# Performance work log

Measured on AMD Instinct MI355X. Metric: run time of the kernel, lower is better.

Reference implementation:

```python
import jax, jax.numpy as jnp
import numpy as np

NEG = -1e12


def setup_inputs() -> dict:
    key = jax.random.key(0)
    ks = jax.random.split(key, 6)
    B, S, D, H = 32, 2048, 1024, 1024  # batch, seq, dec/enc dim, hidden
    last_state = jax.random.normal(ks[0], (B, D), dtype=jnp.float32)
    enc_outputs = jax.random.normal(ks[1], (B, S, D), dtype=jnp.float32)
    attn_masks = jax.random.randint(ks[2], (B, S), 0, 2, dtype=jnp.int32)
    W = jax.random.normal(ks[3], (H, 2 * D), dtype=jnp.float32) * 0.02
    b = jax.random.normal(ks[4], (H,), dtype=jnp.float32) * 0.02
    V = jax.random.normal(ks[5], (H,), dtype=jnp.float32)
    return {"last_state": last_state, "enc_outputs": enc_outputs,
            "attn_masks": attn_masks, "W": W, "b": b, "V": V}


def reference(last_state, enc_outputs, attn_masks, W, b, V):
    # Split W to avoid materializing the [B,S,2D] concat:
    # concat([h, e]) @ W.T == h @ Wh.T + e @ We.T
    D = last_state.shape[-1]
    Wh, We = W[:, :D], W[:, D:]
    # hidden part: [B,H], broadcast over seq
    h_part = jnp.einsum('bd,hd->bh', last_state, Wh)  # [B,H]
    e_part = jnp.einsum('bsd,hd->bsh', enc_outputs, We)  # [B,S,H]
    sim = jnp.tanh(h_part[:, None, :] + e_part + b)  # [B,S,H]
    scores = jnp.einsum('bsh,h->bs', sim, V)  # [B,S]
    scores = jnp.where(attn_masks != 1, jnp.float32(NEG), scores)
    attn_weights = jax.nn.softmax(scores, axis=1)  # [B,S]
    context = jnp.einsum('bs,bsd->bd', attn_weights, enc_outputs)  # [B,D]
    return context, attn_weights, scores
```

## Files before the change

kernel.cpp:

```cpp
#include <hip/hip_runtime.h>
#include <math.h>
#include <stdint.h>

#define B_ 32
#define S_ 2048
#define D_ 1024
#define H_ 1024
#define NEGV -1000000000000.0f

typedef __attribute__((ext_vector_type(8))) short bf16x8;
typedef __attribute__((ext_vector_type(8))) _Float16 f16x8;
typedef __attribute__((ext_vector_type(4))) float f32x4;

static __device__ __forceinline__ unsigned short f2bf(float x) {
    union { float f; unsigned u; } v; v.f = x;
    unsigned r = v.u + 0x7FFF + ((v.u >> 16) & 1);
    return (unsigned short)(r >> 16);
}
static __device__ __forceinline__ float bf2f(unsigned short h) {
    union { float f; unsigned u; } v; v.u = ((unsigned)h) << 16; return v.f;
}
static __device__ __forceinline__ unsigned short f2h(float x) {
    _Float16 h = (_Float16)x; unsigned short u;
    __builtin_memcpy(&u, &h, 2); return u;
}
static __device__ __forceinline__ float h2f(unsigned short u) {
    _Float16 h; __builtin_memcpy(&h, &u, 2); return (float)h;
}
static __device__ __forceinline__ float tanh_fast(float x) {
    float e = __expf(2.f * x);
    return 1.f - 2.f / (e + 1.f);
}
static __device__ __forceinline__ void gl_lds16(unsigned short* lds, const unsigned short* g) {
    __builtin_amdgcn_global_load_lds(
        (const __attribute__((address_space(1))) unsigned int*)(const void*)g,
        (__attribute__((address_space(3))) unsigned int*)(void*)lds,
        16, 0, 0);
}

__global__ __launch_bounds__(256) void k_W_f16(const float* __restrict__ W,
                                               unsigned short* __restrict__ out) {
    int idx = blockIdx.x * 256 + threadIdx.x;
    int h = idx >> 7, kc = idx & 127;
    const float* src = W + (size_t)h * (2 * D_) + D_ + kc * 8;
    float4 a = *(const float4*)src;
    float4 c4 = *(const float4*)(src + 4);
    float v[8] = {a.x, a.y, a.z, a.w, c4.x, c4.y, c4.z, c4.w};
    unsigned short t[8];
#pragma unroll
    for (int j = 0; j < 8; ++j) t[j] = f2h(v[j]);
    uint4 w;
    w.x = t[0] | ((unsigned)t[1] << 16); w.y = t[2] | ((unsigned)t[3] << 16);
    w.z = t[4] | ((unsigned)t[5] << 16); w.w = t[6] | ((unsigned)t[7] << 16);
    int g = kc >> 3, cc = kc & 7;
    int dst = g * 64 + ((cc ^ (h & 7)) << 3);
    *(uint4*)(out + (size_t)h * D_ + dst) = w;
}

__global__ __launch_bounds__(256) void k_hpart(const float* __restrict__ ls,
                                               const float* __restrict__ W,
                                               float* __restrict__ hp) {
    int bh = blockIdx.x * 256 + threadIdx.x;
    int b = bh >> 10, h = bh & 1023;
    const float* lsr = ls + b * D_;
    const float* wr  = W + (size_t)h * (2 * D_);
    float acc = 0.f;
#pragma unroll 4
    for (int d = 0; d < D_; d += 4) {
        float4 a = *(const float4*)(lsr + d);
        float4 w = *(const float4*)(wr + d);
        acc += a.x * w.x + a.y * w.y + a.z * w.z + a.w * w.w;
    }
    hp[bh] = acc;
}

__global__ __launch_bounds__(512, 2) void k_scores_fused(
    const float* __restrict__ enc,
    const unsigned short* __restrict__ Wf16,
    const float* __restrict__ hp, const float* __restrict__ bias,
    const float* __restrict__ V, float* __restrict__ spart)
{
    extern __shared__ unsigned short smem[];
    unsigned short* smemA = smem;
    unsigned short* smemB = smem + 32768;

    const int tid  = threadIdx.x;
    const int lane = tid & 63, wid = tid >> 6;
    const int wm = wid >> 2, wn = wid & 3;
    const int l15 = lane & 15, lhi = lane >> 4;

    const int bid  = blockIdx.x;
    const int wgid = (bid & 7) * 128 + (bid >> 3);
    const int mt = wgid >> 2, nt = wgid & 3;
    const int m0 = mt * 256;
    const int nt256 = nt * 256;
    const int b = m0 >> 11;

    const size_t boff = (size_t)(nt256 + wid * 16 + (lane >> 3)) * D_ + (lane & 7) * 8;
    const int ldsw = wid * 1024;

    f32x4 acc[8][4];
#pragma unroll
    for (int i = 0; i < 8; ++i)
#pragma unroll
        for (int j = 0; j < 4; ++j)
            acc[i][j] = (f32x4){0.f, 0.f, 0.f, 0.f};

    const int swz = l15 & 7;

    float4 ar0[4], ar1[4];

#define LOAD_A(KOFS) do {                                                           \
    _Pragma("unroll")                                                               \
    for (int s_ = 0; s_ < 4; ++s_) {                                                \
        int p_ = tid + s_ * 512;                                                    \
        int row_ = p_ >> 3, pc_ = p_ & 7;                                           \
        const float* ap_ = enc + (size_t)(m0 + row_) * D_ + (KOFS) + pc_ * 8;       \
        ar0[s_] = *(const float4*)ap_;                                              \
        ar1[s_] = *(const float4*)(ap_ + 4);                                        \
    }                                                                               \
} while (0)
#define WRITE_A(SLOT) do {                                                          \
    _Pragma("unroll")                                                               \
    for (int s_ = 0; s_ < 4; ++s_) {                                                \
        int p_ = tid + s_ * 512;                                                    \
        int row_ = p_ >> 3, pc_ = p_ & 7;                                           \
        float v_[8] = {ar0[s_].x, ar0[s_].y, ar0[s_].z, ar0[s_].w,                  \
                       ar1[s_].x, ar1[s_].y, ar1[s_].z, ar1[s_].w};                 \
        unsigned short t_[8];                                                       \
        _Pragma("unroll")                                                           \
        for (int j_ = 0; j_ < 8; ++j_) t_[j_] = f2h(v_[j_]);                        \
        uint4 w_;                                                                   \
        w_.x = t_[0] | ((unsigned)t_[1] << 16); w_.y = t_[2] | ((unsigned)t_[3] << 16); \
        w_.z = t_[4] | ((unsigned)t_[5] << 16); w_.w = t_[6] | ((unsigned)t_[7] << 16); \
        *(uint4*)&smemA[(SLOT) * 16384 + row_ * 64 + ((pc_ ^ (row_ & 7)) << 3)] = w_; \
    }                                                                               \
} while (0)

#define STAGE_B(SLOT, HALF, KOFS) do {                                              \
    unsigned short* d_ = &smemB[(SLOT) * 16384 + (HALF) * 8192 + ldsw];             \
    const unsigned short* s_ = Wf16 + boff + (size_t)(HALF) * 131072 + (KOFS);      \
    gl_lds16(d_, s_);                                                               \
    gl_lds16(d_ + 512, s_ + 8192);                                                  \
} while (0)

#define LDA(AR, CUR, MH, KS) do {                                                   \
    _Pragma("unroll")                                                               \
    for (int fi_ = 0; fi_ < 4; ++fi_) {                                             \
        int row_ = wm * 128 + (MH) * 64 + fi_ * 16 + l15;                           \
        int ch_  = ((KS) * 4 + lhi) ^ swz;                                          \
        AR[fi_] = *(const f16x8*)&smemA[(CUR) * 16384 + row_ * 64 + ch_ * 8];       \
    }                                                                               \
} while (0)
#define LDB(BR, CUR, KS) do {                                                       \
    _Pragma("unroll")                                                               \
    for (int fi_ = 0; fi_ < 4; ++fi_) {                                             \
        int row_ = wn * 64 + fi_ * 16 + l15;                                        \
        int ch_  = ((KS) * 4 + lhi) ^ swz;                                          \
        BR[fi_] = *(const f16x8*)&smemB[(CUR) * 16384 + row_ * 64 + ch_ * 8];       \
    }                                                                               \
} while (0)
#define MFMA16(AR, BR, MH) do {                                                     \
    __builtin_amdgcn_s_setprio(1);                                                  \
    _Pragma("unroll")                                                               \
    for (int fi_ = 0; fi_ < 4; ++fi_)                                               \
    _Pragma("unroll")                                                               \
        for (int fj_ = 0; fj_ < 4; ++fj_)                                           \
            acc[(MH) * 4 + fi_][fj_] = __builtin_amdgcn_mfma_f32_16x16x32_f16(      \
                AR[fi_], BR[fj_], acc[(MH) * 4 + fi_][fj_], 0, 0, 0);               \
    __builtin_amdgcn_s_setprio(0);                                                  \
} while (0)

    LOAD_A(0);
    STAGE_B(0, 0, 0);
    STAGE_B(0, 1, 0);
    WRITE_A(0);
    __syncthreads();

    f16x8 a[4], bk[4];
#pragma unroll 1
    for (int t = 0; t < 16; ++t) {
        const int cur = t & 1, nxt = cur ^ 1;
        const int kofs = (t + 1) * 64;

        if (t < 15) {
            LOAD_A(kofs);
            STAGE_B(nxt, 0, kofs);
            STAGE_B(nxt, 1, kofs);
        }

#pragma unroll
        for (int ks = 0; ks < 2; ++ks) {
            LDB(bk, cur, ks);
            LDA(a, cur, 0, ks);
            MFMA16(a, bk, 0);
            LDA(a, cur, 1, ks);
            MFMA16(a, bk, 1);
        }

        if (t < 15) WRITE_A(nxt);

        __syncthreads();
    }

    float hb[4], vv[4];
#pragma unroll
    for (int fn = 0; fn < 4; ++fn) {
        int h = nt256 + wn * 64 + fn * 16 + l15;
        hb[fn] = hp[b * H_ + h] + bias[h];
        vv[fn] = V[h];
    }
    float* s_red = (float*)smem;
#pragma unroll
    for (int fm = 0; fm < 8; ++fm)
#pragma unroll
        for (int rg = 0; rg < 4; ++rg) {
            float rs = 0.f;
#pragma unroll
            for (int fn = 0; fn < 4; ++fn)
                rs += tanh_fast(acc[fm][fn][rg] + hb[fn]) * vv[fn];
            rs += __shfl_xor(rs, 1, 16);
            rs += __shfl_xor(rs, 2, 16);
            rs += __shfl_xor(rs, 4, 16);
            rs += __shfl_xor(rs, 8, 16);
            if (l15 == 0)
                s_red[wid * 128 + fm * 16 + lhi * 4 + rg] = rs;
        }
    __syncthreads();
    if (tid < 256) {
        int wmr = tid >> 7, rr = tid & 127;
        float v = s_red[(wmr * 4 + 0) * 128 + rr] + s_red[(wmr * 4 + 1) * 128 + rr]
                + s_red[(wmr * 4 + 2) * 128 + rr] + s_red[(wmr * 4 + 3) * 128 + rr];
        spart[(size_t)nt * 65536 + m0 + tid] = v;
    }
#undef LOAD_A
#undef WRITE_A
#undef STAGE_B
#undef LDA
#undef LDB
#undef MFMA16
}

__global__ __launch_bounds__(256) void k_softmax_fold(const float* __restrict__ spart,
                                                      const int* __restrict__ mask,
                                                      float* __restrict__ scores_out,
                                                      float* __restrict__ weights) {
    __shared__ float red[8];
    int b = blockIdx.x, tid = threadIdx.x;
    float vals[8];
    float mx = -INFINITY;
#pragma unroll
    for (int i = 0; i < 8; ++i) {
        int m = b * S_ + tid + i * 256;
        float s = spart[m] + spart[65536 + m] + spart[131072 + m] + spart[196608 + m];
        s = (mask[m] == 1) ? s : NEGV;
        scores_out[m] = s;
        vals[i] = s;
        mx = fmaxf(mx, s);
    }
    for (int off = 32; off; off >>= 1) mx = fmaxf(mx, __shfl_xor(mx, off, 64));
    int wave = tid >> 6;
    if ((tid & 63) == 0) red[wave] = mx;
    __syncthreads();
    mx = fmaxf(fmaxf(red[0], red[1]), fmaxf(red[2], red[3]));
    float sum = 0.f;
#pragma unroll
    for (int i = 0; i < 8; ++i) {
        vals[i] = expf(vals[i] - mx);
        sum += vals[i];
    }
    for (int off = 32; off; off >>= 1) sum += __shfl_xor(sum, off, 64);
    if ((tid & 63) == 0) red[4 + wave] = sum;
    __syncthreads();
    sum = red[4] + red[5] + red[6] + red[7];
    float inv = 1.f / sum;
#pragma unroll
    for (int i = 0; i < 8; ++i)
        weights[b * S_ + tid + i * 256] = vals[i] * inv;
}

__global__ __launch_bounds__(256) void k_ctx_partial_f32(const float* __restrict__ weights,
                                                         const float* __restrict__ enc,
                                                         float* __restrict__ part) {
    int b = blockIdx.x >> 4;
    int chunk = blockIdx.x & 15;
    int tid = threadIdx.x;
    int d0 = tid * 4;
    float4 acc = {0.f, 0.f, 0.f, 0.f};
    int s0 = chunk * 128;
    const float* wrow = weights + b * S_;
    for (int s = s0; s < s0 + 128; ++s) {
        float w = wrow[s];
        if (w != 0.f) {
            float4 e = *(const float4*)(enc + (size_t)(b * S_ + s) * D_ + d0);
            acc.x += w * e.x; acc.y += w * e.y; acc.z += w * e.z; acc.w += w * e.w;
        }
    }
    *(float4*)(part + (size_t)blockIdx.x * D_ + d0) = acc;
}

__global__ __launch_bounds__(256) void k_ctx_reduce(const float* __restrict__ part,
                                                    float* __restrict__ ctx) {
    int bd = blockIdx.x * 256 + threadIdx.x;
    int b = bd >> 10, d = bd & 1023;
    float acc = 0.f;
#pragma unroll
    for (int c = 0; c < 16; ++c)
        acc += part[(size_t)(b * 16 + c) * D_ + d];
    ctx[bd] = acc;
}

__global__ __launch_bounds__(256) void k_splitW_lin(const float* __restrict__ W,
                                                    unsigned short* __restrict__ hi,
                                                    unsigned short* __restrict__ lo) {
    int idx = blockIdx.x * 256 + threadIdx.x;
    int h = idx >> 7, kc = idx & 127;
    const float* src = W + (size_t)h * (2 * D_) + D_ + kc * 8;
    float4 a = *(const float4*)src;
    float4 c = *(const float4*)(src + 4);
    float v[8] = {a.x, a.y, a.z, a.w, c.x, c.y, c.z, c.w};
    unsigned short th[8], tl[8];
#pragma unroll
    for (int j = 0; j < 8; ++j) {
        th[j] = f2bf(v[j]);
        tl[j] = f2bf(v[j] - bf2f(th[j]));
    }
    uint4 hw, lw;
    hw.x = th[0] | ((unsigned)th[1] << 16); hw.y = th[2] | ((unsigned)th[3] << 16);
    hw.z = th[4] | ((unsigned)th[5] << 16); hw.w = th[6] | ((unsigned)th[7] << 16);
    lw.x = tl[0] | ((unsigned)tl[1] << 16); lw.y = tl[2] | ((unsigned)tl[3] << 16);
    lw.z = tl[4] | ((unsigned)tl[5] << 16); lw.w = tl[6] | ((unsigned)tl[7] << 16);
    *(uint4*)(hi + (size_t)h * D_ + kc * 8) = hw;
    *(uint4*)(lo + (size_t)h * D_ + kc * 8) = lw;
}

__global__ __launch_bounds__(256, 2) void k_scores_mfma_fb(
    const float* __restrict__ enc,
    const unsigned short* __restrict__ Whi,
    const unsigned short* __restrict__ Wlo,
    const float* __restrict__ hp,
    const float* __restrict__ bias,
    const float* __restrict__ V,
    const int* __restrict__ mask,
    float* __restrict__ scores_out)
{
    __shared__ __align__(16) unsigned short smem[4 * 8192];
    unsigned short* sAhi = smem;
    unsigned short* sAlo = smem + 8192;
    unsigned short* sBhi = smem + 16384;
    unsigned short* sBlo = smem + 24576;

    const int tid  = threadIdx.x;
    const int lane = tid & 63, wid = tid >> 6;
    const int wr = wid >> 1, wc = wid & 1;
    const int l15 = lane & 15, lhi = lane >> 4;
    const int m0 = blockIdx.x * 128;
    const int b  = m0 >> 11;

    float rowsum[4][4] = {};
    float4 pa[8];
    uint4  pbh[4], pbl[4];

#define STAGE_LOAD(NB, KB) do {                                            \
    _Pragma("unroll")                                                      \
    for (int i_ = 0; i_ < 4; ++i_) {                                       \
        int c_ = tid + i_ * 256;                                           \
        int r_ = c_ >> 3, kc_ = c_ & 7;                                    \
        const float* ap_ = enc + (size_t)(m0 + r_) * D_ + (KB) * 64 + kc_ * 8; \
        pa[2 * i_]     = *(const float4*)ap_;                              \
        pa[2 * i_ + 1] = *(const float4*)(ap_ + 4);                        \
        size_t bo_ = (size_t)((NB) * 128 + r_) * D_ + (KB) * 64 + kc_ * 8; \
        pbh[i_] = *(const uint4*)(Whi + bo_);                              \
        pbl[i_] = *(const uint4*)(Wlo + bo_);                              \
    }                                                                      \
} while (0)

#define STAGE_WRITE() do {                                                 \
    _Pragma("unroll")                                                      \
    for (int i_ = 0; i_ < 4; ++i_) {                                       \
        int c_ = tid + i_ * 256;                                           \
        int sc_ = c_ ^ ((c_ >> 3) & 7);                                    \
        float vv_[8] = {pa[2*i_].x, pa[2*i_].y, pa[2*i_].z, pa[2*i_].w,    \
                        pa[2*i_+1].x, pa[2*i_+1].y, pa[2*i_+1].z, pa[2*i_+1].w}; \
        unsigned short th_[8], tl_[8];                                     \
        _Pragma("unroll")                                                  \
        for (int j_ = 0; j_ < 8; ++j_) {                                   \
            th_[j_] = f2bf(vv_[j_]);                                       \
            tl_[j_] = f2bf(vv_[j_] - bf2f(th_[j_]));                       \
        }                                                                  \
        uint4 hw_, lw_;                                                    \
        hw_.x = th_[0] | ((unsigned)th_[1] << 16); hw_.y = th_[2] | ((unsigned)th_[3] << 16); \
        hw_.z = th_[4] | ((unsigned)th_[5] << 16); hw_.w = th_[6] | ((unsigned)th_[7] << 16); \
        lw_.x = tl_[0] | ((unsigned)tl_[1] << 16); lw_.y = tl_[2] | ((unsigned)tl_[3] << 16); \
        lw_.z = tl_[4] | ((unsigned)tl_[5] << 16); lw_.w = tl_[6] | ((unsigned)tl_[7] << 16); \
        *(uint4*)&sAhi[sc_ * 8] = hw_;                                     \
        *(uint4*)&sAlo[sc_ * 8] = lw_;                                     \
        *(uint4*)&sBhi[sc_ * 8] = pbh[i_];                                 \
        *(uint4*)&sBlo[sc_ * 8] = pbl[i_];                                 \
    }                                                                      \
} while (0)

    STAGE_LOAD(0, 0);

    for (int nb = 0; nb < 8; ++nb) {
        f32x4 acc[4][4];
#pragma unroll
        for (int i = 0; i < 4; ++i)
#pragma unroll
            for (int j = 0; j < 4; ++j)
                acc[i][j] = (f32x4){0.f, 0.f, 0.f, 0.f};

        for (int kb = 0; kb < 16; ++kb) {
            __syncthreads();
            STAGE_WRITE();
            __syncthreads();
            int nkb = kb + 1, nnb = nb;
            if (nkb == 16) { nkb = 0; nnb = nb + 1; }
            if (nnb < 8) STAGE_LOAD(nnb, nkb);

#pragma unroll
            for (int ks = 0; ks < 2; ++ks) {
                bf16x8 bh[4], bl[4];
#pragma unroll
                for (int fn = 0; fn < 4; ++fn) {
                    int rB = wc * 64 + fn * 16 + l15;
                    int ch = (rB * 8 + ks * 4 + lhi) ^ (rB & 7);
                    bh[fn] = *(const bf16x8*)&sBhi[ch * 8];
                    bl[fn] = *(const bf16x8*)&sBlo[ch * 8];
                }
#pragma unroll
                for (int fm = 0; fm < 4; ++fm) {
                    int rA = wr * 64 + fm * 16 + l15;
                    int ch = (rA * 8 + ks * 4 + lhi) ^ (rA & 7);
                    bf16x8 ah = *(const bf16x8*)&sAhi[ch * 8];
                    bf16x8 al = *(const bf16x8*)&sAlo[ch * 8];
#pragma unroll
                    for (int fn = 0; fn < 4; ++fn) {
                        acc[fm][fn] = __builtin_amdgcn_mfma_f32_16x16x32_bf16(ah, bh[fn], acc[fm][fn], 0, 0, 0);
                        acc[fm][fn] = __builtin_amdgcn_mfma_f32_16x16x32_bf16(ah, bl[fn], acc[fm][fn], 0, 0, 0);
                        acc[fm][fn] = __builtin_amdgcn_mfma_f32_16x16x32_bf16(al, bh[fn], acc[fm][fn], 0, 0, 0);
                    }
                }
            }
        }

        int n0 = nb * 128;
#pragma unroll
        for (int fn = 0; fn < 4; ++fn) {
            int n = n0 + wc * 64 + fn * 16 + l15;
            float hbv = hp[b * H_ + n] + bias[n];
            float vvv = V[n];
#pragma unroll
            for (int fm = 0; fm < 4; ++fm) {
                f32x4 a = acc[fm][fn];
#pragma unroll
                for (int rg = 0; rg < 4; ++rg)
                    rowsum[fm][rg] += tanh_fast(a[rg] + hbv) * vvv;
            }
        }
    }

    __syncthreads();
    float* s_red = (float*)smem;
#pragma unroll
    for (int fm = 0; fm < 4; ++fm)
#pragma unroll
        for (int rg = 0; rg < 4; ++rg) {
            float v = rowsum[fm][rg];
            v += __shfl_xor(v, 1, 16);
            v += __shfl_xor(v, 2, 16);
            v += __shfl_xor(v, 4, 16);
            v += __shfl_xor(v, 8, 16);
            if (l15 == 0)
                s_red[wc * 128 + wr * 64 + fm * 16 + lhi * 4 + rg] = v;
        }
    __syncthreads();
    if (tid < 128) {
        int m = m0 + tid;
        float sc = s_red[tid] + s_red[128 + tid];
        scores_out[m] = (mask[m] == 1) ? sc : NEGV;
    }
#undef STAGE_LOAD
#undef STAGE_WRITE
}

__global__ __launch_bounds__(256) void k_softmax(const float* __restrict__ scores,
                                                 float* __restrict__ weights) {
    __shared__ float red[8];
    int b = blockIdx.x;
    int tid = threadIdx.x;
    const float* srow = scores + b * S_;
    float vals[8];
    float mx = -INFINITY;
#pragma unroll
    for (int i = 0; i < 8; ++i) {
        vals[i] = srow[tid + i * 256];
        mx = fmaxf(mx, vals[i]);
    }
    for (int off = 32; off; off >>= 1) mx = fmaxf(mx, __shfl_xor(mx, off, 64));
    int wave = tid >> 6;
    if ((tid & 63) == 0) red[wave] = mx;
    __syncthreads();
    mx = fmaxf(fmaxf(red[0], red[1]), fmaxf(red[2], red[3]));
    float sum = 0.f;
#pragma unroll
    for (int i = 0; i < 8; ++i) {
        vals[i] = expf(vals[i] - mx);
        sum += vals[i];
    }
    for (int off = 32; off; off >>= 1) sum += __shfl_xor(sum, off, 64);
    if ((tid & 63) == 0) red[4 + wave] = sum;
    __syncthreads();
    sum = red[4] + red[5] + red[6] + red[7];
    float inv = 1.f / sum;
#pragma unroll
    for (int i = 0; i < 8; ++i)
        weights[b * S_ + tid + i * 256] = vals[i] * inv;
}

extern "C" void kernel_launch(void* const* d_in, const int* in_sizes, int n_in,
                              void* d_out, int out_size, void* d_ws, size_t ws_size,
                              hipStream_t stream) {
    const float* ls   = (const float*)d_in[0];
    const float* enc  = (const float*)d_in[1];
    const int*   mask = (const int*)d_in[2];
    const float* W    = (const float*)d_in[3];
    const float* bias = (const float*)d_in[4];
    const float* V    = (const float*)d_in[5];

    float* out     = (float*)d_out;
    float* ctx     = out;
    float* weights = out + 32768;
    float* scores  = out + 98304;

    const size_t need = 2097152ull + 131072ull + 1048576ull + 2097152ull;

    if (ws_size >= need) {
        unsigned short* Wf16 = (unsigned short*)d_ws;
        float* hp    = (float*)(Wf16 + 1048576);
        float* spart = hp + 32768;
        float* part  = spart + 262144;

        hipFuncSetAttribute((const void*)k_scores_fused,
                            hipFuncAttributeMaxDynamicSharedMemorySize, 131072);

        k_W_f16<<<512, 256, 0, stream>>>(W, Wf16);
        k_hpart<<<128, 256, 0, stream>>>(ls, W, hp);
        k_scores_fused<<<1024, 512, 131072, stream>>>(enc, Wf16, hp, bias, V, spart);
        k_softmax_fold<<<32, 256, 0, stream>>>(spart, mask, scores, weights);
        k_ctx_partial_f32<<<512, 256, 0, stream>>>(weights, enc, part);
        k_ctx_reduce<<<128, 256, 0, stream>>>(part, ctx);
    } else {
        unsigned short* Whi = (unsigned short*)d_ws;
        unsigned short* Wlo = Whi + 1048576;
        float* hp   = (float*)(Wlo + 1048576);
        float* part = hp + 32768;

        k_splitW_lin<<<512, 256, 0, stream>>>(W, Whi, Wlo);
        k_hpart<<<128, 256, 0, stream>>>(ls, W, hp);
        k_scores_mfma_fb<<<512, 256, 0, stream>>>(enc, Whi, Wlo, hp, bias, V, mask, scores);
        k_softmax<<<32, 256, 0, stream>>>(scores, weights);
        k_ctx_partial_f32<<<512, 256, 0, stream>>>(weights, enc, part);
        k_ctx_reduce<<<128, 256, 0, stream>>>(part, ctx);
    }
}
```

Before: 256.7 us.

## Restructure scores GEMM into four-phase pipeline with fragment-major LDS layout

The fused scores GEMM main loop is split into four phases. Each phase interleaves LDS fragment reads, global loads of the next A tile, async B staging and MFMA groups, separated by explicit s_barrier, lgkmcnt and vmcnt waits. LDS now holds A and B in a fragment-major layout with no swizzle, so the W conversion kernel writes a linear layout. The goal is to hide global latency behind MFMA work and spread the LDS writes across the loop. The cost is many more barriers per iteration and possible LDS bank conflicts without the XOR swizzle.

```diff
diff --git a/kernel.cpp b/kernel.cpp
--- a/kernel.cpp
+++ b/kernel.cpp
@@ -38,8 +38,8 @@
         16, 0, 0);
 }
 
-__global__ __launch_bounds__(256) void k_W_f16(const float* __restrict__ W,
-                                               unsigned short* __restrict__ out) {
+__global__ __launch_bounds__(256) void k_W_f16_lin(const float* __restrict__ W,
+                                                   unsigned short* __restrict__ out) {
     int idx = blockIdx.x * 256 + threadIdx.x;
     int h = idx >> 7, kc = idx & 127;
     const float* src = W + (size_t)h * (2 * D_) + D_ + kc * 8;
@@ -52,9 +52,7 @@
     uint4 w;
     w.x = t[0] | ((unsigned)t[1] << 16); w.y = t[2] | ((unsigned)t[3] << 16);
     w.z = t[4] | ((unsigned)t[5] << 16); w.w = t[6] | ((unsigned)t[7] << 16);
-    int g = kc >> 3, cc = kc & 7;
-    int dst = g * 64 + ((cc ^ (h & 7)) << 3);
-    *(uint4*)(out + (size_t)h * D_ + dst) = w;
+    *(uint4*)(out + (size_t)h * D_ + kc * 8) = w;
 }
 
 __global__ __launch_bounds__(256) void k_hpart(const float* __restrict__ ls,
@@ -74,7 +72,7 @@
     hp[bh] = acc;
 }
 
-__global__ __launch_bounds__(512, 2) void k_scores_fused(
+__global__ __launch_bounds__(512, 2) void k_scores_4ph(
     const float* __restrict__ enc,
     const unsigned short* __restrict__ Wf16,
     const float* __restrict__ hp, const float* __restrict__ bias,
@@ -96,8 +94,9 @@
     const int nt256 = nt * 256;
     const int b = m0 >> 11;
 
-    const size_t boff = (size_t)(nt256 + wid * 16 + (lane >> 3)) * D_ + (lane & 7) * 8;
-    const int ldsw = wid * 1024;
+    const int arow_base = m0 + wm * 128 + wn * 32;
+    const int brg = wn * 4 + wm * 2;
+    const size_t bsrc_base = (size_t)(nt256 + brg * 16 + l15) * D_ + lhi * 8;
 
     f32x4 acc[8][4];
 #pragma unroll
@@ -106,59 +105,44 @@
         for (int j = 0; j < 4; ++j)
             acc[i][j] = (f32x4){0.f, 0.f, 0.f, 0.f};
 
-    const int swz = l15 & 7;
-
     float4 ar0[4], ar1[4];
 
-#define LOAD_A(KOFS) do {                                                           \
+#define LOAD_A1(S, KOFS) do {                                                       \
+    const float* ap_ = enc + (size_t)(arow_base + ((S) & 1) * 16 + l15) * D_        \
+                     + (KOFS) + (((S) >> 1) * 4 + lhi) * 8;                         \
+    ar0[S] = *(const float4*)ap_;                                                   \
+    ar1[S] = *(const float4*)(ap_ + 4);                                             \
+} while (0)
+#define WRITE_A1(S, SLOT) do {                                                      \
+    float v_[8] = {ar0[S].x, ar0[S].y, ar0[S].z, ar0[S].w,                          \
+                   ar1[S].x, ar1[S].y, ar1[S].z, ar1[S].w};                         \
+    unsigned short t_[8];                                                           \
     _Pragma("unroll")                                                               \
-    for (int s_ = 0; s_ < 4; ++s_) {                                                \
-        int p_ = tid + s_ * 512;                                                    \
-        int row_ = p_ >> 3, pc_ = p_ & 7;                                           \
-        const float* ap_ = enc + (size_t)(m0 + row_) * D_ + (KOFS) + pc_ * 8;       \
-        ar0[s_] = *(const float4*)ap_;                                              \
-        ar1[s_] = *(const float4*)(ap_ + 4);                                        \
-    }                                                                               \
-} while (0)
-#define WRITE_A(SLOT) do {                                                          \
-    _Pragma("unroll")                                                               \
-    for (int s_ = 0; s_ < 4; ++s_) {                                                \
-        int p_ = tid + s_ * 512;                                                    \
-        int row_ = p_ >> 3, pc_ = p_ & 7;                                           \
-        float v_[8] = {ar0[s_].x, ar0[s_].y, ar0[s_].z, ar0[s_].w,                  \
-                       ar1[s_].x, ar1[s_].y, ar1[s_].z, ar1[s_].w};                 \
-        unsigned short t_[8];                                                       \
-        _Pragma("unroll")                                                           \
-        for (int j_ = 0; j_ < 8; ++j_) t_[j_] = f2h(v_[j_]);                        \
-        uint4 w_;                                                                   \
-        w_.x = t_[0] | ((unsigned)t_[1] << 16); w_.y = t_[2] | ((unsigned)t_[3] << 16); \
-        w_.z = t_[4] | ((unsigned)t_[5] << 16); w_.w = t_[6] | ((unsigned)t_[7] << 16); \
-        *(uint4*)&smemA[(SLOT) * 16384 + row_ * 64 + ((pc_ ^ (row_ & 7)) << 3)] = w_; \
-    }                                                                               \
-} while (0)
-
-#define STAGE_B(SLOT, HALF, KOFS) do {                                              \
-    unsigned short* d_ = &smemB[(SLOT) * 16384 + (HALF) * 8192 + ldsw];             \
-    const unsigned short* s_ = Wf16 + boff + (size_t)(HALF) * 131072 + (KOFS);      \
-    gl_lds16(d_, s_);                                                               \
-    gl_lds16(d_ + 512, s_ + 8192);                                                  \
+    for (int j_ = 0; j_ < 8; ++j_) t_[j_] = f2h(v_[j_]);                            \
+    uint4 w_;                                                                       \
+    w_.x = t_[0] | ((unsigned)t_[1] << 16); w_.y = t_[2] | ((unsigned)t_[3] << 16); \
+    w_.z = t_[4] | ((unsigned)t_[5] << 16); w_.w = t_[6] | ((unsigned)t_[7] << 16); \
+    *(uint4*)&smemA[(SLOT) * 16384 + (wm * 8 + wn * 2 + ((S) & 1)) * 1024           \
+                    + (((S) >> 1) * 4 + lhi) * 128 + l15 * 8] = w_;                 \
+} while (0)
+#define STAGE_B(SLOT, KS, KOFS) do {                                                \
+    gl_lds16(&smemB[(SLOT) * 16384 + brg * 1024 + (KS) * 512],                      \
+             Wf16 + bsrc_base + (KOFS) + (KS) * 32);                                \
+    gl_lds16(&smemB[(SLOT) * 16384 + (brg + 1) * 1024 + (KS) * 512],                \
+             Wf16 + bsrc_base + 16 * D_ + (KOFS) + (KS) * 32);                      \
 } while (0)
 
 #define LDA(AR, CUR, MH, KS) do {                                                   \
     _Pragma("unroll")                                                               \
-    for (int fi_ = 0; fi_ < 4; ++fi_) {                                             \
-        int row_ = wm * 128 + (MH) * 64 + fi_ * 16 + l15;                           \
-        int ch_  = ((KS) * 4 + lhi) ^ swz;                                          \
-        AR[fi_] = *(const f16x8*)&smemA[(CUR) * 16384 + row_ * 64 + ch_ * 8];       \
-    }                                                                               \
+    for (int fi_ = 0; fi_ < 4; ++fi_)                                               \
+        AR[fi_] = *(const f16x8*)&smemA[(CUR) * 16384                               \
+            + (wm * 8 + (MH) * 4 + fi_) * 1024 + ((KS) * 4 + lhi) * 128 + l15 * 8]; \
 } while (0)
 #define LDB(BR, CUR, KS) do {                                                       \
     _Pragma("unroll")                                                               \
-    for (int fi_ = 0; fi_ < 4; ++fi_) {                                             \
-        int row_ = wn * 64 + fi_ * 16 + l15;                                        \
-        int ch_  = ((KS) * 4 + lhi) ^ swz;                                          \
-        BR[fi_] = *(const f16x8*)&smemB[(CUR) * 16384 + row_ * 64 + ch_ * 8];       \
-    }                                                                               \
+    for (int fi_ = 0; fi_ < 4; ++fi_)                                               \
+        BR[fi_] = *(const f16x8*)&smemB[(CUR) * 16384                               \
+            + (wn * 4 + fi_) * 1024 + ((KS) * 4 + lhi) * 128 + l15 * 8];            \
 } while (0)
 #define MFMA16(AR, BR, MH) do {                                                     \
     __builtin_amdgcn_s_setprio(1);                                                  \
@@ -171,10 +155,16 @@
     __builtin_amdgcn_s_setprio(0);                                                  \
 } while (0)
 
-    LOAD_A(0);
+#define BARRIER() asm volatile("s_barrier" ::: "memory")
+#define LGKM0()  do { asm volatile("s_waitcnt lgkmcnt(0)" ::: "memory");            \
+                      __builtin_amdgcn_sched_barrier(0); } while (0)
+#define VMC(N)   do { asm volatile("s_waitcnt vmcnt(" #N ")" ::: "memory");         \
+                      __builtin_amdgcn_sched_barrier(0); } while (0)
+
+    LOAD_A1(0, 0); LOAD_A1(1, 0); LOAD_A1(2, 0); LOAD_A1(3, 0);
+    WRITE_A1(0, 0); WRITE_A1(1, 0); WRITE_A1(2, 0); WRITE_A1(3, 0);
     STAGE_B(0, 0, 0);
     STAGE_B(0, 1, 0);
-    WRITE_A(0);
     __syncthreads();
 
     f16x8 a[4], bk[4];
@@ -182,25 +172,37 @@
     for (int t = 0; t < 16; ++t) {
         const int cur = t & 1, nxt = cur ^ 1;
         const int kofs = (t + 1) * 64;
-
-        if (t < 15) {
-            LOAD_A(kofs);
-            STAGE_B(nxt, 0, kofs);
-            STAGE_B(nxt, 1, kofs);
-        }
-
-#pragma unroll
-        for (int ks = 0; ks < 2; ++ks) {
-            LDB(bk, cur, ks);
-            LDA(a, cur, 0, ks);
-            MFMA16(a, bk, 0);
-            LDA(a, cur, 1, ks);
-            MFMA16(a, bk, 1);
-        }
-
-        if (t < 15) WRITE_A(nxt);
-
-        __syncthreads();
+        const bool pf = (t < 15);
+
+        LDB(bk, cur, 0);
+        LDA(a, cur, 0, 0);
+        if (pf) { LOAD_A1(0, kofs); LOAD_A1(1, kofs); }
+        BARRIER(); LGKM0();
+        MFMA16(a, bk, 0);
+        BARRIER();
+
+        LDA(a, cur, 1, 0);
+        if (pf) { LOAD_A1(2, kofs); LOAD_A1(3, kofs); }
+        BARRIER(); LGKM0();
+        MFMA16(a, bk, 1);
+        VMC(8);
+        BARRIER();
+
+        if (pf) { WRITE_A1(0, nxt); WRITE_A1(1, nxt); }
+        LDB(bk, cur, 1);
+        LDA(a, cur, 0, 1);
+        if (pf) STAGE_B(nxt, 0, kofs);
+        BARRIER(); LGKM0();
+        MFMA16(a, bk, 0);
+        BARRIER();
+
+        if (pf) { WRITE_A1(2, nxt); WRITE_A1(3, nxt); }
+        LDA(a, cur, 1, 1);
+        if (pf) STAGE_B(nxt, 1, kofs);
+        BARRIER(); LGKM0();
+        MFMA16(a, bk, 1);
+        VMC(2);
+        BARRIER();
     }
 
     float hb[4], vv[4];
@@ -233,12 +235,15 @@
                 + s_red[(wmr * 4 + 2) * 128 + rr] + s_red[(wmr * 4 + 3) * 128 + rr];
         spart[(size_t)nt * 65536 + m0 + tid] = v;
     }
-#undef LOAD_A
-#undef WRITE_A
+#undef LOAD_A1
+#undef WRITE_A1
 #undef STAGE_B
 #undef LDA
 #undef LDB
 #undef MFMA16
+#undef BARRIER
+#undef LGKM0
+#undef VMC
 }
 
 __global__ __launch_bounds__(256) void k_softmax_fold(const float* __restrict__ spart,
@@ -541,12 +546,12 @@
         float* spart = hp + 32768;
         float* part  = spart + 262144;
 
-        hipFuncSetAttribute((const void*)k_scores_fused,
+        hipFuncSetAttribute((const void*)k_scores_4ph,
                             hipFuncAttributeMaxDynamicSharedMemorySize, 131072);
 
-        k_W_f16<<<512, 256, 0, stream>>>(W, Wf16);
+        k_W_f16_lin<<<512, 256, 0, stream>>>(W, Wf16);
         k_hpart<<<128, 256, 0, stream>>>(ls, W, hp);
-        k_scores_fused<<<1024, 512, 131072, stream>>>(enc, Wf16, hp, bias, V, spart);
+        k_scores_4ph<<<1024, 512, 131072, stream>>>(enc, Wf16, hp, bias, V, spart);
         k_softmax_fold<<<32, 256, 0, stream>>>(spart, mask, scores, weights);
         k_ctx_partial_f32<<<512, 256, 0, stream>>>(weights, enc, part);
         k_ctx_reduce<<<128, 256, 0, stream>>>(part, ctx);
```

Measured after the change: 329.1 us. 28.2% more time.
